# Kernel tuning notes

Hardware: AMD Instinct MI355X
Metric: run time of the kernel (lower is better)

The kernel has to match this reference:

```python
import jax, jax.numpy as jnp
import numpy as np

HEADS = 8
DIM_HEAD = 64

def setup_inputs() -> dict:
    key = jax.random.key(0)
    ks = jax.random.split(key, 5)
    B, n, dim = 128, 512, 256
    inner = HEADS * DIM_HEAD  # 512
    return {
        'x': jax.random.normal(ks[0], (B, n, dim), dtype=jnp.float32),
        'Wq': jax.random.normal(ks[1], (dim, inner), dtype=jnp.float32) * (dim ** -0.5),
        'Wkv': jax.random.normal(ks[2], (dim, 2 * inner), dtype=jnp.float32) * (dim ** -0.5),
        'Wo': jax.random.normal(ks[3], (inner, dim), dtype=jnp.float32) * (inner ** -0.5),
        'bo': jnp.zeros((dim,), dtype=jnp.float32),
        'tie_attn_dim': 64,
    }

def reference(x, Wq, Wkv, Wo, bo, tie_attn_dim):
    h, dh = HEADS, DIM_HEAD
    B, n, dim = x.shape
    r = tie_attn_dim
    b = B // r
    q = x @ Wq                      # [B, n, h*dh]
    kv = x @ Wkv                    # [B, n, 2*h*dh] (self-attention: context = x)
    k, v = jnp.split(kv, 2, axis=-1)
    # '(b r) n (h d) -> b r h n d'
    def to_tied(t):
        return t.reshape(b, r, n, h, dh).transpose(0, 1, 3, 2, 4)
    q, k, v = map(to_tied, (q, k, v))
    scale = (dh ** -0.5) * (r ** -0.5)
    # tied row attention: reduce over MSA rows r and head dim d
    dots = jnp.einsum('brhid,brhjd->bhij', q, k) * scale  # [b, h, n, n]
    attn = jax.nn.softmax(dots, axis=-1)
    out = jnp.einsum('bhij,brhjd->brhid', attn, v)        # [b, r, h, n, dh]
    # 'b r h n d -> (b r) n (h d)'
    out = out.transpose(0, 1, 3, 2, 4).reshape(B, n, h * dh)
    return out @ Wo + bo
```

## Files before the change

### kernel.cpp

```cpp
#include <hip/hip_runtime.h>

typedef unsigned short u16;
typedef __attribute__((ext_vector_type(8))) short bf16x8;
typedef __attribute__((ext_vector_type(4))) float f32x4;

struct __align__(8) U16x4 { u16 a, b, c, d; };

__device__ __forceinline__ u16 f2bf(float f) {
  union { float f; unsigned int u; } cv; cv.f = f;
  unsigned int u = cv.u;
  unsigned int r = (u + 0x7fffu + ((u >> 16) & 1u)) >> 16;
  return (u16)r;
}

__device__ __forceinline__ void gld16(const u16* g, u16* l) {
  __builtin_amdgcn_global_load_lds((const __attribute__((address_space(1))) void*)g,
                                   (__attribute__((address_space(3))) void*)l, 16, 0, 0);
}

__global__ void conv_k(const float* __restrict__ x, u16* __restrict__ xbf) {
  size_t i = ((size_t)blockIdx.x * 256 + threadIdx.x) * 8;
  u16 tmp[8];
  #pragma unroll
  for (int j = 0; j < 8; j++) tmp[j] = f2bf(x[i + j]);
  *(bf16x8*)&xbf[i] = *(const bf16x8*)&tmp[0];
}

__global__ void prep_k(const float* __restrict__ Wq, const float* __restrict__ Wkv,
                       const float* __restrict__ Wo, u16* __restrict__ WT1,
                       u16* __restrict__ WoT) {
  int idx = blockIdx.x * 256 + threadIdx.x;
  if (idx < 1536 * 256) {
    int c = idx >> 8, k = idx & 255;
    WT1[idx] = (c < 512) ? f2bf(Wq[(size_t)k * 512 + c])
                         : f2bf(Wkv[(size_t)k * 1024 + (c - 512)]);
  }
  if (idx < 256 * 512) {
    int nn = idx >> 9, kk = idx & 511;
    WoT[idx] = f2bf(Wo[(size_t)kk * 256 + nn]);
  }
}

template<int KIND>
__global__ void __launch_bounds__(256, 4) gemm_k(
    const u16* __restrict__ A, const u16* __restrict__ B,
    u16* __restrict__ C, u16* __restrict__ C2,
    float* __restrict__ SF, const float* __restrict__ bias,
    int aux0, int nk32) {
  __shared__ __align__(16) u16 lsm[16384];
  u16* lAq[2] = { lsm,        lsm + 4096 };
  u16* lBq[2] = { lsm + 8192, lsm + 12288 };

  const int tid  = threadIdx.x;
  const int bid  = blockIdx.x;
  const int lane = tid & 63;
  const int wv   = tid >> 6;
  const int l15  = lane & 15;
  const int quad = lane >> 4;
  const int mq   = (wv & 1) * 64;
  const int nq   = (wv >> 1) * 64;

  int m0, n0, NK2, kb0 = 0;
  int s = 0, p = 0;
  if constexpr (KIND == 1) {
    int nwg = aux0 * 12;
    int per = nwg >> 3;
    int sw  = (bid & 7) * per + (bid >> 3);
    m0 = (sw / 12) * 128; n0 = (sw % 12) * 128; NK2 = 4;
  } else if constexpr (KIND == 2) {
    int npS = aux0;
    n0 = (bid & 3) * 128; m0 = ((bid >> 2) & 3) * 128;
    p = (bid >> 4) & ((1 << npS) - 1); s = bid >> (4 + npS);
    NK2 = nk32 >> 1; kb0 = s * nk32;
  } else if constexpr (KIND == 3) {
    n0 = (bid & 31) * 128; m0 = ((bid >> 5) & 3) * 128; p = bid >> 7; NK2 = 8;
  } else {
    n0 = (bid & 1) * 128; m0 = (bid >> 1) * 128; NK2 = 8;
  }

  f32x4 acc[4][4];
  #pragma unroll
  for (int i = 0; i < 4; i++)
    #pragma unroll
    for (int j = 0; j < 4; j++)
      #pragma unroll
      for (int g = 0; g < 4; g++) acc[i][j][g] = 0.f;

  const int ar0 = tid >> 2;
  const int ac0 = (tid & 3) * 8;

  for (int t = 0; t < NK2; t++) {
    #pragma unroll
    for (int q = 0; q < 2; q++) {
      const int kb = kb0 + 2 * t + q;
      size_t aBase, bBase; int aRS, bRS;
      if constexpr (KIND == 1) {
        aBase = (size_t)m0 * 256 + kb * 32; aRS = 256;
        bBase = (size_t)n0 * 256 + kb * 32; bRS = 256;
      } else if constexpr (KIND == 2) {
        int bt = p >> 3, hl = p & 7;
        int r = kb >> 1, dlo = (kb & 1) * 32;
        size_t rowblk = (size_t)bt * 32768 + (size_t)r * 512;
        aBase = (rowblk + m0) * 1024 + hl * 64 + dlo;        aRS = 1024;
        bBase = (rowblk + n0) * 1024 + 512 + hl * 64 + dlo;  bRS = 1024;
      } else if constexpr (KIND == 3) {
        aBase = ((size_t)p * 512 + m0) * 512 + kb * 32;   aRS = 512;
        bBase = ((size_t)p * 4096 + n0) * 512 + kb * 32;  bRS = 512;
      } else {
        int bt = m0 >> 15, h = kb >> 1, dlo = (kb & 1) * 32;
        aBase = ((size_t)(bt * 8 + h) * 512 + (m0 & 511)) * 4096
                + ((m0 >> 9) & 63) * 64 + dlo;
        aRS = 4096;
        bBase = (size_t)n0 * 512 + kb * 32; bRS = 512;
      }
      gld16(A + aBase + (size_t)ar0 * aRS + ac0,        &lAq[q][tid * 8]);
      gld16(A + aBase + (size_t)(ar0 + 64) * aRS + ac0, &lAq[q][(tid + 256) * 8]);
      gld16(B + bBase + (size_t)ar0 * bRS + ac0,        &lBq[q][tid * 8]);
      gld16(B + bBase + (size_t)(ar0 + 64) * bRS + ac0, &lBq[q][(tid + 256) * 8]);
    }
    __syncthreads();

    #pragma unroll
    for (int q = 0; q < 2; q++) {
      bf16x8 af[4], bfr[4];
      #pragma unroll
      for (int mi = 0; mi < 4; mi++)
        af[mi] = *(const bf16x8*)&lAq[q][(mq + mi * 16 + l15) * 32 + quad * 8];
      #pragma unroll
      for (int ni = 0; ni < 4; ni++)
        bfr[ni] = *(const bf16x8*)&lBq[q][(nq + ni * 16 + l15) * 32 + quad * 8];
      #pragma unroll
      for (int mi = 0; mi < 4; mi++)
        #pragma unroll
        for (int ni = 0; ni < 4; ni++)
          acc[mi][ni] = __builtin_amdgcn_mfma_f32_16x16x32_bf16(af[mi], bfr[ni], acc[mi][ni], 0, 0, 0);
    }
    __syncthreads();
  }

  if constexpr (KIND == 1 || KIND == 3) {
    if (KIND == 3 || n0 < 1024) {
      #pragma unroll
      for (int ps = 0; ps < 2; ps++) {
        if ((mq >> 6) == ps) {
          #pragma unroll
          for (int mi = 0; mi < 4; mi++)
            #pragma unroll
            for (int ni = 0; ni < 4; ni++) {
              int lr = mi * 16 + quad * 4;
              int lc = nq + ni * 16 + l15;
              #pragma unroll
              for (int g = 0; g < 4; g++)
                lsm[(lr + g) * 136 + lc] = f2bf(acc[mi][ni][g]);
            }
        }
        __syncthreads();
        #pragma unroll
        for (int it = 0; it < 4; it++) {
          int idx = tid + it * 256;
          int lr = idx >> 4, c = (idx & 15) * 8;
          int gm = m0 + ps * 64 + lr;
          size_t gaddr;
          if constexpr (KIND == 1) gaddr = (size_t)gm * 1024 + n0 + c;
          else                     gaddr = ((size_t)p * 512 + gm) * 4096 + n0 + c;
          *(bf16x8*)&C[gaddr] = *(const bf16x8*)&lsm[lr * 136 + c];
        }
        __syncthreads();
      }
    } else {
      #pragma unroll
      for (int ps = 0; ps < 2; ps++) {
        if ((nq >> 6) == ps) {
          #pragma unroll
          for (int mi = 0; mi < 4; mi++)
            #pragma unroll
            for (int ni = 0; ni < 4; ni++) {
              int lrn = ni * 16 + l15;
              int lcm = mq + mi * 16 + quad * 4;
              U16x4 pk;
              pk.a = f2bf(acc[mi][ni][0]); pk.b = f2bf(acc[mi][ni][1]);
              pk.c = f2bf(acc[mi][ni][2]); pk.d = f2bf(acc[mi][ni][3]);
              *(U16x4*)&lsm[lrn * 136 + lcm] = pk;
            }
        }
        __syncthreads();
        int bt2 = m0 >> 15;
        int r  = (m0 >> 9) & 63;
        int jb = (m0 & 511);
        #pragma unroll
        for (int it = 0; it < 4; it++) {
          int idx = tid + it * 256;
          int lr = idx >> 4, c = (idx & 15) * 8;
          int cc = (n0 - 1024) + ps * 64 + lr;
          int h = cc >> 6, d = cc & 63;
          size_t gaddr = ((size_t)(bt2 * 8 + h) * 4096 + r * 64 + d) * 512 + jb + c;
          *(bf16x8*)&C2[gaddr] = *(const bf16x8*)&lsm[lr * 136 + c];
        }
        __syncthreads();
      }
    }
  } else {
    float* lsf = (float*)lsm;
    #pragma unroll
    for (int ps = 0; ps < 4; ps++) {
      if ((mq >> 6) == (ps >> 1)) {
        int miA = (ps & 1) * 2;
        #pragma unroll
        for (int mm = 0; mm < 2; mm++) {
          int mi = miA + mm;
          #pragma unroll
          for (int ni = 0; ni < 4; ni++) {
            int lr = mm * 16 + quad * 4;
            int lc = nq + ni * 16 + l15;
            #pragma unroll
            for (int g = 0; g < 4; g++)
              lsf[(lr + g) * 132 + lc] = acc[mi][ni][g];
          }
        }
      }
      __syncthreads();
      #pragma unroll
      for (int it = 0; it < 4; it++) {
        int idx = tid + it * 256;
        int lr = idx >> 5, c = (idx & 31) * 4;
        int gm = m0 + ps * 32 + lr;
        f32x4 v = *(const f32x4*)&lsf[lr * 132 + c];
        if constexpr (KIND == 2) {
          int npS = aux0;
          *(f32x4*)&SF[((size_t)((s << npS) + p) * 512 + gm) * 512 + n0 + c] = v;
        } else {
          f32x4 bo4 = *(const f32x4*)&bias[n0 + c];
          v[0] += bo4[0]; v[1] += bo4[1]; v[2] += bo4[2]; v[3] += bo4[3];
          *(f32x4*)&SF[(size_t)gm * 256 + n0 + c] = v;
        }
      }
      __syncthreads();
    }
  }
}

__global__ void softmax_k(const float* __restrict__ SP, u16* __restrict__ P,
                          int nsplit, int np) {
  int bid = blockIdx.x;
  int p = bid >> 9, i = bid & 511;
  int t = threadIdx.x;
  size_t rowbase = ((size_t)p * 512 + i) * 512;
  float v0 = 0.f, v1 = 0.f;
  for (int ss = 0; ss < nsplit; ss++) {
    size_t off = (size_t)ss * np * 512 * 512;
    float2 u = *(const float2*)&SP[off + rowbase + 2 * t];
    v0 += u.x; v1 += u.y;
  }
  const float scale = 1.0f / 64.0f;
  v0 *= scale; v1 *= scale;

  int wv = t >> 6, ln = t & 63;
  float m = fmaxf(v0, v1);
  for (int o = 32; o > 0; o >>= 1) m = fmaxf(m, __shfl_down(m, o));
  __shared__ float sred[4];
  if (ln == 0) sred[wv] = m;
  __syncthreads();
  m = fmaxf(fmaxf(sred[0], sred[1]), fmaxf(sred[2], sred[3]));

  float e0 = expf(v0 - m), e1 = expf(v1 - m);
  float sum = e0 + e1;
  for (int o = 32; o > 0; o >>= 1) sum += __shfl_down(sum, o);
  __shared__ float sred2[4];
  if (ln == 0) sred2[wv] = sum;
  __syncthreads();
  float inv = 1.0f / (sred2[0] + sred2[1] + sred2[2] + sred2[3]);

  unsigned int pk = (unsigned int)f2bf(e0 * inv)
                  | ((unsigned int)f2bf(e1 * inv) << 16);
  *(unsigned int*)&P[rowbase + 2 * t] = pk;
}

extern "C" void kernel_launch(void* const* d_in, const int* in_sizes, int n_in,
                              void* d_out, int out_size, void* d_ws, size_t ws_size,
                              hipStream_t stream) {
  (void)in_sizes; (void)n_in; (void)out_size;
  const float* x   = (const float*)d_in[0];
  const float* Wq  = (const float*)d_in[1];
  const float* Wkv = (const float*)d_in[2];
  const float* Wo  = (const float*)d_in[3];
  const float* bo  = (const float*)d_in[4];
  float* out = (float*)d_out;

  const size_t MB = 1024ull * 1024ull;
  const int ns_m = 2;
  bool merged = (ws_size >= 235 * MB);

  char* ws = (char*)d_ws;
  size_t off = 0;
  u16* WT1 = (u16*)(ws + off); off += (size_t)1536 * 256 * 2;
  u16* WoT = (u16*)(ws + off); off += (size_t)256 * 512 * 2;

  prep_k<<<dim3(1536), dim3(256), 0, stream>>>(Wq, Wkv, Wo, WT1, WoT);

  if (merged) {
    const int np = 16, npS = 4, ns = ns_m;
    u16* QK = (u16*)(ws + off); off += (size_t)65536 * 1024 * 2;
    u16* OT = QK;
    u16* VT = (u16*)(ws + off); off += (size_t)np * 4096 * 512 * 2;
    u16* Pb = (u16*)(ws + off); off += (size_t)np * 512 * 512 * 2;
    char* XS = ws + off;
    u16* xbf = (u16*)XS;
    float* SP = (float*)XS;

    conv_k<<<dim3(8192), dim3(256), 0, stream>>>(x, xbf);
    gemm_k<1><<<dim3(512 * 12), dim3(256), 0, stream>>>(xbf, WT1, QK, VT,
                                                        nullptr, nullptr, 512, 0);
    gemm_k<2><<<dim3(ns * np * 16), dim3(256), 0, stream>>>(QK, QK, nullptr, nullptr,
                                                            SP, nullptr, npS, 128 / ns);
    softmax_k<<<dim3(np * 512), dim3(256), 0, stream>>>(SP, Pb, ns, np);
    gemm_k<3><<<dim3(np * 128), dim3(256), 0, stream>>>(Pb, VT, OT, nullptr,
                                                        nullptr, nullptr, 0, 0);
    gemm_k<4><<<dim3(1024), dim3(256), 0, stream>>>(OT, WoT, nullptr, nullptr,
                                                    out, bo, 0, 0);
  } else {
    const int np = 8, npS = 3;
    u16* QKb = (u16*)(ws + off); off += (size_t)32768 * 1024 * 2;
    u16* OTb = QKb;
    u16* VTb = (u16*)(ws + off); off += (size_t)np * 4096 * 512 * 2;
    u16* Pb  = (u16*)(ws + off); off += (size_t)np * 512 * 512 * 2;
    char* XS = ws + off;
    u16* xbf = (u16*)XS;
    float* SPb = (float*)XS;
    size_t rem = (ws_size > off) ? (ws_size - off) : 0;
    int ns = 2;
    while (ns > 1 && (size_t)ns * np * 512 * 512 * 4 > rem) ns >>= 1;

    for (int bt = 0; bt < 2; bt++) {
      const float* xb = x + (size_t)bt * 32768 * 256;
      float* outb = out + (size_t)bt * 32768 * 256;
      conv_k<<<dim3(4096), dim3(256), 0, stream>>>(xb, xbf);
      gemm_k<1><<<dim3(256 * 12), dim3(256), 0, stream>>>(xbf, WT1, QKb, VTb,
                                                          nullptr, nullptr, 256, 0);
      gemm_k<2><<<dim3(ns * np * 16), dim3(256), 0, stream>>>(QKb, QKb, nullptr, nullptr,
                                                              SPb, nullptr, npS, 128 / ns);
      softmax_k<<<dim3(np * 512), dim3(256), 0, stream>>>(SPb, Pb, ns, np);
      gemm_k<3><<<dim3(np * 128), dim3(256), 0, stream>>>(Pb, VTb, OTb, nullptr,
                                                          nullptr, nullptr, 0, 0);
      gemm_k<4><<<dim3(512), dim3(256), 0, stream>>>(OTb, WoT, nullptr, nullptr,
                                                     outb, bo, 0, 0);
    }
  }
}
```

Baseline: 357.0 us.

## Software-pipeline GEMM main loop with double-buffered LDS prefetch

The GEMM k-loop used to load two 32-wide k-blocks into LDS, synchronise, compute both, then synchronise again. It now loads one k-block ahead into the alternate LDS buffer while running MFMAs on the current one, with a single barrier per k-block. The aim is to overlap global-to-LDS loads with matrix math instead of serialising them. The barrier count per k element stays the same, but each barrier now covers half as much compute, and the overlap depends on the barrier waiting for outstanding async LDS loads.

Measured after the change: 353.3 us. Within noise of the previous version (-1.0%).

```diff
diff --git a/kernel.cpp b/kernel.cpp
--- a/kernel.cpp
+++ b/kernel.cpp
@@ -48,8 +48,6 @@
     float* __restrict__ SF, const float* __restrict__ bias,
     int aux0, int nk32) {
   __shared__ __align__(16) u16 lsm[16384];
-  u16* lAq[2] = { lsm,        lsm + 4096 };
-  u16* lBq[2] = { lsm + 8192, lsm + 12288 };
 
   const int tid  = threadIdx.x;
   const int bid  = blockIdx.x;
@@ -89,54 +87,63 @@
   const int ar0 = tid >> 2;
   const int ac0 = (tid & 3) * 8;
 
-  for (int t = 0; t < NK2; t++) {
-    #pragma unroll
-    for (int q = 0; q < 2; q++) {
-      const int kb = kb0 + 2 * t + q;
-      size_t aBase, bBase; int aRS, bRS;
-      if constexpr (KIND == 1) {
-        aBase = (size_t)m0 * 256 + kb * 32; aRS = 256;
-        bBase = (size_t)n0 * 256 + kb * 32; bRS = 256;
-      } else if constexpr (KIND == 2) {
-        int bt = p >> 3, hl = p & 7;
-        int r = kb >> 1, dlo = (kb & 1) * 32;
-        size_t rowblk = (size_t)bt * 32768 + (size_t)r * 512;
-        aBase = (rowblk + m0) * 1024 + hl * 64 + dlo;        aRS = 1024;
-        bBase = (rowblk + n0) * 1024 + 512 + hl * 64 + dlo;  bRS = 1024;
-      } else if constexpr (KIND == 3) {
-        aBase = ((size_t)p * 512 + m0) * 512 + kb * 32;   aRS = 512;
-        bBase = ((size_t)p * 4096 + n0) * 512 + kb * 32;  bRS = 512;
-      } else {
-        int bt = m0 >> 15, h = kb >> 1, dlo = (kb & 1) * 32;
-        aBase = ((size_t)(bt * 8 + h) * 512 + (m0 & 511)) * 4096
-                + ((m0 >> 9) & 63) * 64 + dlo;
-        aRS = 4096;
-        bBase = (size_t)n0 * 512 + kb * 32; bRS = 512;
-      }
-      gld16(A + aBase + (size_t)ar0 * aRS + ac0,        &lAq[q][tid * 8]);
-      gld16(A + aBase + (size_t)(ar0 + 64) * aRS + ac0, &lAq[q][(tid + 256) * 8]);
-      gld16(B + bBase + (size_t)ar0 * bRS + ac0,        &lBq[q][tid * 8]);
-      gld16(B + bBase + (size_t)(ar0 + 64) * bRS + ac0, &lBq[q][(tid + 256) * 8]);
-    }
+#define STAGE_KB(kb_, bi_)                                                     \
+  do {                                                                         \
+    const int kb = (kb_);                                                      \
+    size_t aBase, bBase; int aRS, bRS;                                         \
+    if constexpr (KIND == 1) {                                                 \
+      aBase = (size_t)m0 * 256 + kb * 32; aRS = 256;                           \
+      bBase = (size_t)n0 * 256 + kb * 32; bRS = 256;                           \
+    } else if constexpr (KIND == 2) {                                          \
+      int bt = p >> 3, hl = p & 7;                                             \
+      int r = kb >> 1, dlo = (kb & 1) * 32;                                    \
+      size_t rowblk = (size_t)bt * 32768 + (size_t)r * 512;                    \
+      aBase = (rowblk + m0) * 1024 + hl * 64 + dlo;        aRS = 1024;         \
+      bBase = (rowblk + n0) * 1024 + 512 + hl * 64 + dlo;  bRS = 1024;         \
+    } else if constexpr (KIND == 3) {                                          \
+      aBase = ((size_t)p * 512 + m0) * 512 + kb * 32;   aRS = 512;             \
+      bBase = ((size_t)p * 4096 + n0) * 512 + kb * 32;  bRS = 512;             \
+    } else {                                                                   \
+      int bt = m0 >> 15, h = kb >> 1, dlo = (kb & 1) * 32;                     \
+      aBase = ((size_t)(bt * 8 + h) * 512 + (m0 & 511)) * 4096                 \
+              + ((m0 >> 9) & 63) * 64 + dlo;                                   \
+      aRS = 4096;                                                              \
+      bBase = (size_t)n0 * 512 + kb * 32; bRS = 512;                           \
+    }                                                                          \
+    u16* lA_ = lsm + (bi_) * 4096;                                             \
+    u16* lB_ = lsm + 8192 + (bi_) * 4096;                                      \
+    gld16(A + aBase + (size_t)ar0 * aRS + ac0,        &lA_[tid * 8]);          \
+    gld16(A + aBase + (size_t)(ar0 + 64) * aRS + ac0, &lA_[(tid + 256) * 8]);  \
+    gld16(B + bBase + (size_t)ar0 * bRS + ac0,        &lB_[tid * 8]);          \
+    gld16(B + bBase + (size_t)(ar0 + 64) * bRS + ac0, &lB_[(tid + 256) * 8]);  \
+  } while (0)
+
+  const int NKtot = NK2 * 2;
+  STAGE_KB(kb0, 0);
+  __syncthreads();
+
+  for (int step = 0; step < NKtot; ++step) {
+    const int cur = step & 1;
+    if (step + 1 < NKtot) STAGE_KB(kb0 + step + 1, cur ^ 1);
+
+    const u16* lA = lsm + cur * 4096;
+    const u16* lB = lsm + 8192 + cur * 4096;
+    bf16x8 af[4], bfr[4];
+    #pragma unroll
+    for (int mi = 0; mi < 4; mi++)
+      af[mi] = *(const bf16x8*)&lA[(mq + mi * 16 + l15) * 32 + quad * 8];
+    #pragma unroll
+    for (int ni = 0; ni < 4; ni++)
+      bfr[ni] = *(const bf16x8*)&lB[(nq + ni * 16 + l15) * 32 + quad * 8];
+    #pragma unroll
+    for (int mi = 0; mi < 4; mi++)
+      #pragma unroll
+      for (int ni = 0; ni < 4; ni++)
+        acc[mi][ni] = __builtin_amdgcn_mfma_f32_16x16x32_bf16(af[mi], bfr[ni], acc[mi][ni], 0, 0, 0);
+
     __syncthreads();
-
-    #pragma unroll
-    for (int q = 0; q < 2; q++) {
-      bf16x8 af[4], bfr[4];
-      #pragma unroll
-      for (int mi = 0; mi < 4; mi++)
-        af[mi] = *(const bf16x8*)&lAq[q][(mq + mi * 16 + l15) * 32 + quad * 8];
-      #pragma unroll
-      for (int ni = 0; ni < 4; ni++)
-        bfr[ni] = *(const bf16x8*)&lBq[q][(nq + ni * 16 + l15) * 32 + quad * 8];
-      #pragma unroll
-      for (int mi = 0; mi < 4; mi++)
-        #pragma unroll
-        for (int ni = 0; ni < 4; ni++)
-          acc[mi][ni] = __builtin_amdgcn_mfma_f32_16x16x32_bf16(af[mi], bfr[ni], acc[mi][ni], 0, 0, 0);
-    }
-    __syncthreads();
-  }
+  }
+#undef STAGE_KB
 
   if constexpr (KIND == 1 || KIND == 3) {
     if (KIND == 3 || n0 < 1024) {
```
